# Optimization experiments

Measured on AMD Instinct MI355X. Metric: run time of the kernel, lower is better.

Reference implementation:

```python
import jax, jax.numpy as jnp
import numpy as np

B, H, W, C = 128, 56, 56, 96
N = H * W  # tokens


def setup_inputs() -> dict:
    key = jax.random.key(0)
    k1, k2 = jax.random.split(key)
    x = jax.random.normal(k1, (B, N, C), dtype=jnp.float32)
    # original inits to 0.02 * ones; use small random values for a non-trivial baseline
    weight_c = jax.random.uniform(k2, (N, C // 2 + 1, 2), dtype=jnp.float32) * 0.02
    return {"x": x, "weight_c": weight_c}


def reference(x, weight_c):
    # x: [B, N, C]; rfft along channel dim, per-token complex filter, irfft back
    c = x.shape[2]
    xf = jnp.fft.rfft(x.astype(jnp.float32), axis=2, norm="ortho")  # [B, N, C//2+1] complex
    w = jax.lax.complex(weight_c[..., 0], weight_c[..., 1])          # [N, C//2+1] complex
    y = xf * w  # broadcast over batch
    return jnp.fft.irfft(y, n=c, axis=2, norm="ortho")  # [B, N, C]
```

## Files before the change

### kernel.cpp

```cpp
#include <hip/hip_runtime.h>
#include <hip/hip_bf16.h>

#ifndef M_PI
#define M_PI 3.14159265358979323846
#endif

static constexpr int B_ = 128;
static constexpr int N_ = 3136;
static constexpr int C_ = 96;
static constexpr int NC = N_ * C_;
static constexpr int PITCH = 104;

typedef short short8 __attribute__((ext_vector_type(8)));
typedef float float4v __attribute__((ext_vector_type(4)));

static __device__ __forceinline__ unsigned short f2bf(float f) {
  __hip_bfloat16 b = __float2bfloat16(f);
  return *reinterpret_cast<unsigned short*>(&b);
}

__global__ __launch_bounds__(128) void gf_hbuild_kernel(
    const float* __restrict__ wc, unsigned short* __restrict__ wsB) {
  const int n = blockIdx.x;
  const int tid = threadIdx.x;
  __shared__ float wsh[98];
  __shared__ float cs[96], sn[96];
  __shared__ unsigned short hlb[96];

  if (tid < 98) wsh[tid] = wc[n * 98 + tid];
  if (tid < 96) {
    float s, c;
    sincosf((float)(2.0 * M_PI / 96.0) * (float)tid, &s, &c);
    cs[tid] = c;
    sn[tid] = s;
  }
  __syncthreads();

  if (tid < 96) {
    const int c = tid;
    float acc = wsh[0] + ((c & 1) ? -wsh[96] : wsh[96]);
    int idx = c;
    for (int k = 1; k <= 47; ++k) {
      acc += 2.0f * (wsh[2 * k] * cs[idx] - wsh[2 * k + 1] * sn[idx]);
      idx += c;
      if (idx >= 96) idx -= 96;
    }
    hlb[c] = f2bf(acc * (1.0f / 96.0f));
  }
  __syncthreads();

  unsigned int* out = reinterpret_cast<unsigned int*>(wsB + (size_t)n * 1536);
  for (int e = tid; e < 768; e += 128) {
    const int s = e / 96;
    const int jp = e - s * 96;
    const int a = 288 - (2 * jp + s);
    const unsigned int lo = hlb[a % 96];
    const unsigned int hi = hlb[(a - 1) % 96];
    out[e] = lo | (hi << 16);
  }
}

__global__ __launch_bounds__(256, 4) void gf_mfma2_kernel(
    const float* __restrict__ x, const unsigned short* __restrict__ wsB,
    float* __restrict__ y) {
  const int n = blockIdx.x;
  const int tid = threadIdx.x;
  const int wv = tid >> 6;
  const int l = tid & 63;
  const int lrow = l & 15;
  const int lk = l >> 4;

  float4 v0[2][3], v1[2][3];
#pragma unroll
  for (int mt = 0; mt < 2; ++mt) {
    const float* xp =
        x + (size_t)((wv * 2 + mt) * 16 + lrow) * NC + n * C_ + lk * 8;
#pragma unroll
    for (int kq = 0; kq < 3; ++kq) {
      v0[mt][kq] = *reinterpret_cast<const float4*>(xp + kq * 32);
      v1[mt][kq] = *reinterpret_cast<const float4*>(xp + kq * 32 + 4);
    }
  }
  short8 afr[2][3];
#pragma unroll
  for (int mt = 0; mt < 2; ++mt)
#pragma unroll
    for (int kq = 0; kq < 3; ++kq) {
      short8 a;
      a[0] = (short)f2bf(v0[mt][kq].x);
      a[1] = (short)f2bf(v0[mt][kq].y);
      a[2] = (short)f2bf(v0[mt][kq].z);
      a[3] = (short)f2bf(v0[mt][kq].w);
      a[4] = (short)f2bf(v1[mt][kq].x);
      a[5] = (short)f2bf(v1[mt][kq].y);
      a[6] = (short)f2bf(v1[mt][kq].z);
      a[7] = (short)f2bf(v1[mt][kq].w);
      afr[mt][kq] = a;
    }

  const int M0 = 96 + lk * 8 - lrow;
  const unsigned short* wb0 =
      wsB + (size_t)n * 1536 + (M0 & 7) * 192 + (M0 & ~7);

  float4v acc[2][6];
#pragma unroll
  for (int mt = 0; mt < 2; ++mt)
#pragma unroll
    for (int nt = 0; nt < 6; ++nt)
#pragma unroll
      for (int i = 0; i < 4; ++i) acc[mt][nt][i] = 0.0f;

#pragma unroll
  for (int nt = 0; nt < 6; ++nt) {
#pragma unroll
    for (int kq = 0; kq < 3; ++kq) {
      const short8 bfr =
          *reinterpret_cast<const short8*>(wb0 + kq * 32 - nt * 16);
      acc[0][nt] = __builtin_amdgcn_mfma_f32_16x16x32_bf16(afr[0][kq], bfr,
                                                           acc[0][nt], 0, 0, 0);
      acc[1][nt] = __builtin_amdgcn_mfma_f32_16x16x32_bf16(afr[1][kq], bfr,
                                                           acc[1][nt], 0, 0, 0);
    }
  }

#pragma unroll
  for (int mt = 0; mt < 2; ++mt) {
    const int brow0 = (wv * 2 + mt) * 16 + lk * 4;
#pragma unroll
    for (int i = 0; i < 4; ++i) {
      float* yp = y + (size_t)(brow0 + i) * NC + (size_t)n * C_;
#pragma unroll
      for (int nt = 0; nt < 6; ++nt) {
        yp[nt * 16 + lrow] = acc[mt][nt][i];
      }
    }
  }
}

__global__ __launch_bounds__(256, 3) void gf_mfma_kernel(
    const float* __restrict__ x, const float* __restrict__ wc,
    float* __restrict__ y) {
  const int n = blockIdx.x;
  const int tid = threadIdx.x;

  __shared__ __align__(16) unsigned short Asm[128 * PITCH];
  __shared__ __align__(16) unsigned short Ht[96 * PITCH];
  __shared__ float wsh[98];
  __shared__ float cs[96];
  __shared__ float sn[96];
  __shared__ unsigned short hrevd[192];

  float4 xv[12];
  const float* xbase = x + (size_t)n * C_;
#pragma unroll
  for (int p = 0; p < 12; ++p) {
    const int fidx = p * 256 + tid;
    const int b = fidx / 24;
    const int t4 = fidx - b * 24;
    xv[p] = *reinterpret_cast<const float4*>(xbase + (size_t)b * NC + 4 * t4);
  }

  if (tid < 98) wsh[tid] = wc[n * 98 + tid];
  if (tid < 96) {
    float s, c;
    sincosf((float)(2.0 * M_PI / 96.0) * (float)tid, &s, &c);
    cs[tid] = c;
    sn[tid] = s;
  }
  __syncthreads();

  if (tid < 96) {
    const int c = tid;
    float acc = wsh[0] + ((c & 1) ? -wsh[96] : wsh[96]);
    int idx = c;
    for (int k = 1; k <= 47; ++k) {
      acc += 2.0f * (wsh[2 * k] * cs[idx] - wsh[2 * k + 1] * sn[idx]);
      idx += c;
      if (idx >= 96) idx -= 96;
    }
    const unsigned short hb = f2bf(acc * (1.0f / 96.0f));
    hrevd[96 - c] = hb;
    hrevd[(c == 0) ? 0 : (192 - c)] = hb;
  }

#pragma unroll
  for (int p = 0; p < 12; ++p) {
    const int fidx = p * 256 + tid;
    const int b = fidx / 24;
    const int t4 = fidx - b * 24;
    ushort4 o;
    o.x = f2bf(xv[p].x);
    o.y = f2bf(xv[p].y);
    o.z = f2bf(xv[p].z);
    o.w = f2bf(xv[p].w);
    *reinterpret_cast<ushort4*>(&Asm[b * PITCH + 4 * t4]) = o;
  }
  __syncthreads();

  for (int j = tid; j < 96 * 48; j += 256) {
    const int c = j / 48;
    const int kp = j - c * 48;
    const int m = 96 - c + 2 * kp;
    const unsigned int lo = hrevd[m];
    const unsigned int hi = hrevd[m + 1];
    *reinterpret_cast<unsigned int*>(&Ht[c * PITCH + 2 * kp]) = lo | (hi << 16);
  }
  __syncthreads();

  const int wv = tid >> 6;
  const int l = tid & 63;
  const int lrow = l & 15;
  const int lk = l >> 4;

  float4v acc[2][6];
#pragma unroll
  for (int mt = 0; mt < 2; ++mt)
#pragma unroll
    for (int nt = 0; nt < 6; ++nt)
#pragma unroll
      for (int i = 0; i < 4; ++i) acc[mt][nt][i] = 0.0f;

  short8 afr[2][3];
#pragma unroll
  for (int mt = 0; mt < 2; ++mt)
#pragma unroll
    for (int kq = 0; kq < 3; ++kq)
      afr[mt][kq] = *reinterpret_cast<const short8*>(
          &Asm[((wv * 2 + mt) * 16 + lrow) * PITCH + kq * 32 + lk * 8]);

#pragma unroll
  for (int nt = 0; nt < 6; ++nt) {
#pragma unroll
    for (int kq = 0; kq < 3; ++kq) {
      const short8 bfr = *reinterpret_cast<const short8*>(
          &Ht[(nt * 16 + lrow) * PITCH + kq * 32 + lk * 8]);
      acc[0][nt] = __builtin_amdgcn_mfma_f32_16x16x32_bf16(afr[0][kq], bfr,
                                                           acc[0][nt], 0, 0, 0);
      acc[1][nt] = __builtin_amdgcn_mfma_f32_16x16x32_bf16(afr[1][kq], bfr,
                                                           acc[1][nt], 0, 0, 0);
    }
  }

#pragma unroll
  for (int mt = 0; mt < 2; ++mt) {
    const int brow0 = (wv * 2 + mt) * 16 + lk * 4;
#pragma unroll
    for (int i = 0; i < 4; ++i) {
      float* yp = y + (size_t)(brow0 + i) * NC + (size_t)n * C_;
#pragma unroll
      for (int nt = 0; nt < 6; ++nt) {
        yp[nt * 16 + lrow] = acc[mt][nt][i];
      }
    }
  }
}

extern "C" void kernel_launch(void* const* d_in, const int* in_sizes, int n_in,
                              void* d_out, int out_size, void* d_ws, size_t ws_size,
                              hipStream_t stream) {
  const float* x = (const float*)d_in[0];
  const float* wc = (const float*)d_in[1];
  float* y = (float*)d_out;

  const size_t need = (size_t)N_ * 1536 * sizeof(unsigned short);
  if (ws_size >= need) {
    unsigned short* wsB = (unsigned short*)d_ws;
    hipLaunchKernelGGL(gf_hbuild_kernel, dim3(N_), dim3(128), 0, stream, wc, wsB);
    hipLaunchKernelGGL(gf_mfma2_kernel, dim3(N_), dim3(256), 0, stream, x, wsB, y);
  } else {
    hipLaunchKernelGGL(gf_mfma_kernel, dim3(N_), dim3(256), 0, stream, x, wc, y);
  }
}
```

Before: 298.5 us.

## Swap MFMA operands for vectorized nontemporal stores and remap token-to-block order

Swaps the A and B operands of the MFMA so the accumulator holds channels per lane rather than batch rows. Each lane can then write its output as a contiguous float4 nontemporal store instead of scattered scalar stores. It also permutes the block-to-token mapping across 8 groups, which changes how blocks are spread across XCDs and cache slices. The operand swap depends on the H fragment layout still giving the correct transposed product.

```diff
diff --git a/kernel.cpp b/kernel.cpp
--- a/kernel.cpp
+++ b/kernel.cpp
@@ -19,9 +19,13 @@
   return *reinterpret_cast<unsigned short*>(&b);
 }
 
+static __device__ __forceinline__ int token_of_block(int bid) {
+  return (bid & 7) * 392 + (bid >> 3);
+}
+
 __global__ __launch_bounds__(128) void gf_hbuild_kernel(
     const float* __restrict__ wc, unsigned short* __restrict__ wsB) {
-  const int n = blockIdx.x;
+  const int n = token_of_block(blockIdx.x);
   const int tid = threadIdx.x;
   __shared__ float wsh[98];
   __shared__ float cs[96], sn[96];
@@ -60,10 +64,10 @@
   }
 }
 
-__global__ __launch_bounds__(256, 4) void gf_mfma2_kernel(
+__global__ __launch_bounds__(256, 4) void gf_mfma3_kernel(
     const float* __restrict__ x, const unsigned short* __restrict__ wsB,
     float* __restrict__ y) {
-  const int n = blockIdx.x;
+  const int n = token_of_block(blockIdx.x);
   const int tid = threadIdx.x;
   const int wv = tid >> 6;
   const int l = tid & 63;
@@ -72,30 +76,30 @@
 
   float4 v0[2][3], v1[2][3];
 #pragma unroll
-  for (int mt = 0; mt < 2; ++mt) {
+  for (int bt = 0; bt < 2; ++bt) {
     const float* xp =
-        x + (size_t)((wv * 2 + mt) * 16 + lrow) * NC + n * C_ + lk * 8;
-#pragma unroll
-    for (int kq = 0; kq < 3; ++kq) {
-      v0[mt][kq] = *reinterpret_cast<const float4*>(xp + kq * 32);
-      v1[mt][kq] = *reinterpret_cast<const float4*>(xp + kq * 32 + 4);
-    }
-  }
-  short8 afr[2][3];
-#pragma unroll
-  for (int mt = 0; mt < 2; ++mt)
+        x + (size_t)((wv * 2 + bt) * 16 + lrow) * NC + n * C_ + lk * 8;
+#pragma unroll
+    for (int kq = 0; kq < 3; ++kq) {
+      v0[bt][kq] = *reinterpret_cast<const float4*>(xp + kq * 32);
+      v1[bt][kq] = *reinterpret_cast<const float4*>(xp + kq * 32 + 4);
+    }
+  }
+  short8 xfr[2][3];
+#pragma unroll
+  for (int bt = 0; bt < 2; ++bt)
 #pragma unroll
     for (int kq = 0; kq < 3; ++kq) {
       short8 a;
-      a[0] = (short)f2bf(v0[mt][kq].x);
-      a[1] = (short)f2bf(v0[mt][kq].y);
-      a[2] = (short)f2bf(v0[mt][kq].z);
-      a[3] = (short)f2bf(v0[mt][kq].w);
-      a[4] = (short)f2bf(v1[mt][kq].x);
-      a[5] = (short)f2bf(v1[mt][kq].y);
-      a[6] = (short)f2bf(v1[mt][kq].z);
-      a[7] = (short)f2bf(v1[mt][kq].w);
-      afr[mt][kq] = a;
+      a[0] = (short)f2bf(v0[bt][kq].x);
+      a[1] = (short)f2bf(v0[bt][kq].y);
+      a[2] = (short)f2bf(v0[bt][kq].z);
+      a[3] = (short)f2bf(v0[bt][kq].w);
+      a[4] = (short)f2bf(v1[bt][kq].x);
+      a[5] = (short)f2bf(v1[bt][kq].y);
+      a[6] = (short)f2bf(v1[bt][kq].z);
+      a[7] = (short)f2bf(v1[bt][kq].w);
+      xfr[bt][kq] = a;
     }
 
   const int M0 = 96 + lk * 8 - lrow;
@@ -104,35 +108,33 @@
 
   float4v acc[2][6];
 #pragma unroll
-  for (int mt = 0; mt < 2; ++mt)
+  for (int bt = 0; bt < 2; ++bt)
 #pragma unroll
     for (int nt = 0; nt < 6; ++nt)
 #pragma unroll
-      for (int i = 0; i < 4; ++i) acc[mt][nt][i] = 0.0f;
+      for (int i = 0; i < 4; ++i) acc[bt][nt][i] = 0.0f;
 
 #pragma unroll
   for (int nt = 0; nt < 6; ++nt) {
 #pragma unroll
     for (int kq = 0; kq < 3; ++kq) {
-      const short8 bfr =
+      const short8 hfr =
           *reinterpret_cast<const short8*>(wb0 + kq * 32 - nt * 16);
-      acc[0][nt] = __builtin_amdgcn_mfma_f32_16x16x32_bf16(afr[0][kq], bfr,
+      acc[0][nt] = __builtin_amdgcn_mfma_f32_16x16x32_bf16(hfr, xfr[0][kq],
                                                            acc[0][nt], 0, 0, 0);
-      acc[1][nt] = __builtin_amdgcn_mfma_f32_16x16x32_bf16(afr[1][kq], bfr,
+      acc[1][nt] = __builtin_amdgcn_mfma_f32_16x16x32_bf16(hfr, xfr[1][kq],
                                                            acc[1][nt], 0, 0, 0);
     }
   }
 
 #pragma unroll
-  for (int mt = 0; mt < 2; ++mt) {
-    const int brow0 = (wv * 2 + mt) * 16 + lk * 4;
-#pragma unroll
-    for (int i = 0; i < 4; ++i) {
-      float* yp = y + (size_t)(brow0 + i) * NC + (size_t)n * C_;
-#pragma unroll
-      for (int nt = 0; nt < 6; ++nt) {
-        yp[nt * 16 + lrow] = acc[mt][nt][i];
-      }
+  for (int bt = 0; bt < 2; ++bt) {
+    float* yp = y + (size_t)((wv * 2 + bt) * 16 + lrow) * NC +
+                (size_t)n * C_ + lk * 4;
+#pragma unroll
+    for (int nt = 0; nt < 6; ++nt) {
+      __builtin_nontemporal_store(
+          acc[bt][nt], reinterpret_cast<float4v*>(yp + nt * 16));
     }
   }
 }
@@ -266,7 +268,7 @@
   if (ws_size >= need) {
     unsigned short* wsB = (unsigned short*)d_ws;
     hipLaunchKernelGGL(gf_hbuild_kernel, dim3(N_), dim3(128), 0, stream, wc, wsB);
-    hipLaunchKernelGGL(gf_mfma2_kernel, dim3(N_), dim3(256), 0, stream, x, wsB, y);
+    hipLaunchKernelGGL(gf_mfma3_kernel, dim3(N_), dim3(256), 0, stream, x, wsB, y);
   } else {
     hipLaunchKernelGGL(gf_mfma_kernel, dim3(N_), dim3(256), 0, stream, x, wc, y);
   }
```

Measured after the change: 300.4 us. About the same (+0.6%).
